# Performance work log

Measured on AMD Instinct MI355X. Metric: run time of the kernel, lower is better.

The kernel has to match this reference:

```python
import jax, jax.numpy as jnp
import numpy as np


def _apply_rope(t, cos, sin):
    # t: [b, s, h, d]; cos/sin: [s, d//2]; interleaved complex rotation
    b, s, h, d = t.shape
    tr = t.reshape(b, s, h, d // 2, 2)
    a, bb = tr[..., 0], tr[..., 1]
    c = cos[None, :, None, :]
    si = sin[None, :, None, :]
    out_r = a * c - bb * si
    out_i = a * si + bb * c
    return jnp.stack([out_r, out_i], axis=-1).reshape(b, s, h, d)


def setup_inputs() -> dict:
    key = jax.random.key(0)
    ks = jax.random.split(key, 10)
    B, S, D = 4, 512, 4096
    H, HKV, HD = 32, 8, 128
    START = 512
    wscale = 0.02  # keep activations in sane range
    x = jax.random.normal(ks[0], (B, S, D), dtype=jnp.float32)
    wq = jax.random.normal(ks[1], (H * HD, D), dtype=jnp.float32) * wscale
    wk = jax.random.normal(ks[2], (HKV * HD, D), dtype=jnp.float32) * wscale
    wv = jax.random.normal(ks[3], (HKV * HD, D), dtype=jnp.float32) * wscale
    wo = jax.random.normal(ks[4], (D, H * HD), dtype=jnp.float32) * wscale
    # RoPE angles for absolute positions [START, START+S)
    theta = 500000.0
    inv_freq = 1.0 / (theta ** (np.arange(0, HD, 2, dtype=np.float32) / HD))
    pos = np.arange(START, START + S, dtype=np.float32)
    ang = pos[:, None] * inv_freq[None, :]  # [S, HD//2]
    freqs_cos = jnp.asarray(np.cos(ang), dtype=jnp.float32)
    freqs_sin = jnp.asarray(np.sin(ang), dtype=jnp.float32)
    cache_k = jax.random.normal(ks[5], (B, START, HKV, HD), dtype=jnp.float32)
    cache_v = jax.random.normal(ks[6], (B, START, HKV, HD), dtype=jnp.float32)
    return {"x": x, "wq": wq, "wk": wk, "wv": wv, "wo": wo,
            "freqs_cos": freqs_cos, "freqs_sin": freqs_sin,
            "cache_k": cache_k, "cache_v": cache_v, "start_pos": START}


def reference(x, wq, wk, wv, wo, freqs_cos, freqs_sin, cache_k, cache_v, start_pos):
    B, S, D = x.shape
    H = wq.shape[0] // 128
    HKV = wk.shape[0] // 128
    HD = 128
    n_rep = H // HKV
    # QKV projections (Linear: y = x @ W^T)
    xq = jnp.einsum('bsd,ed->bse', x, wq).reshape(B, S, H, HD)
    xk = jnp.einsum('bsd,ed->bse', x, wk).reshape(B, S, HKV, HD)
    xv = jnp.einsum('bsd,ed->bse', x, wv).reshape(B, S, HKV, HD)
    # rotary embedding on new q/k
    xq = _apply_rope(xq, freqs_cos, freqs_sin)
    xk = _apply_rope(xk, freqs_cos, freqs_sin)
    # append new k/v to cache -> total kv length T = start_pos + S
    keys = jnp.concatenate([cache_k, xk], axis=1)    # [B, T, HKV, HD]
    values = jnp.concatenate([cache_v, xv], axis=1)  # [B, T, HKV, HD]
    # GQA: repeat kv heads (repeat_interleave along head dim)
    keys = jnp.repeat(keys, n_rep, axis=2)      # [B, T, H, HD]
    values = jnp.repeat(values, n_rep, axis=2)  # [B, T, H, HD]
    scores = jnp.einsum('bqhd,bkhd->bhqk', xq, keys) / jnp.sqrt(jnp.float32(HD))
    # causal mask: query abs pos start_pos+i attends to kv pos <= start_pos+i
    T = start_pos + S
    q_pos = start_pos + jnp.arange(S)
    k_pos = jnp.arange(T)
    mask = k_pos[None, :] <= q_pos[:, None]  # [S, T]
    scores = jnp.where(mask[None, None, :, :], scores, -jnp.inf)
    probs = jax.nn.softmax(scores.astype(jnp.float32), axis=-1).astype(x.dtype)
    out = jnp.einsum('bhqk,bkhd->bqhd', probs, values).reshape(B, S, H * HD)
    return jnp.einsum('bse,de->bsd', out, wo)
```

## Files before the change

### kernel.cpp

```cpp
#include <hip/hip_runtime.h>
#include <hip/hip_bf16.h>


#define B_ 4
#define S_ 512
#define D_ 4096
#define H_ 32
#define HKV_ 8
#define HD_ 128
#define T_ 1024
#define M_ 2048
#define NQKV_ 6144

typedef __attribute__((ext_vector_type(8))) short bf16x8;
typedef __attribute__((ext_vector_type(4))) float f32x4;

#define GLOAD_LDS16(g, l)                                                     \
  __builtin_amdgcn_global_load_lds(                                           \
      (const __attribute__((address_space(1))) void*)(g),                     \
      (__attribute__((address_space(3))) void*)(l), 16, 0, 0)

__global__ void cvt_f32_bf16(const float* __restrict__ in,
                             __hip_bfloat16* __restrict__ out, long n) {
  long i = ((long)blockIdx.x * blockDim.x + threadIdx.x) * 4;
  if (i >= n) return;
  float4 v = *(const float4*)(in + i);
  __hip_bfloat16 t[4] = {__float2bfloat16(v.x), __float2bfloat16(v.y),
                         __float2bfloat16(v.z), __float2bfloat16(v.w)};
  *(uint2*)(out + i) = *(const uint2*)t;
}

__global__ __launch_bounds__(512, 2) void gemm256(
    const __hip_bfloat16* __restrict__ A, const __hip_bfloat16* __restrict__ B,
    float* __restrict__ C, int M, int N, int K, long ldA, long ldB, long ldC) {
  const int nbx = N >> 8;
  const int nwg = nbx * (M >> 8);
  const int lin = blockIdx.x + nbx * blockIdx.y;
  const int cpx = nwg >> 3;
  const int swz = (lin & 7) * cpx + (lin >> 3);
  const int m0 = (swz / nbx) << 8;
  const int n0 = (swz - (swz / nbx) * nbx) << 8;

  const int tid = threadIdx.x;
  const int w = tid >> 6, l = tid & 63;
  const int wm = w >> 2, wn = w & 3;
  const int lr = l & 15, lq = l >> 4;

  __shared__ __align__(16) __hip_bfloat16 smem[8][8192];

  const int rS = w * 16 + (l >> 2);
  const int cS = (l & 3) ^ ((rS >> 1) & 3);
  const __hip_bfloat16* gA = A + (long)(m0 + rS) * ldA + cS * 8;
  const __hip_bfloat16* gB = B + (long)(n0 + rS) * ldB + cS * 8;
  const long stA = 128 * ldA, stB = 128 * ldB;
  const int wofs = w * 512;

  const int cR = (lq ^ ((lr >> 1) & 3)) * 8;
  const int aOff = (wm * 128 + lr) * 32 + cR;
  const int bOff = (wn * 64 + lr) * 32 + cR;

  f32x4 acc[8][4];
#pragma unroll
  for (int i = 0; i < 8; i++)
#pragma unroll
    for (int j = 0; j < 4; j++) acc[i][j] = f32x4{0.f, 0.f, 0.f, 0.f};

  const int nkt = K >> 6;

#define STAGE_A(buf, kh, ko)                                  \
  {                                                           \
    const __hip_bfloat16* g_ = gA + (ko) + (kh) * 32;         \
    __hip_bfloat16* d_ = &smem[(buf) * 4 + (kh)][wofs];       \
    GLOAD_LDS16(g_, d_);                                      \
    GLOAD_LDS16(g_ + stA, d_ + 4096);                         \
  }
#define STAGE_B(buf, kh, ko)                                  \
  {                                                           \
    const __hip_bfloat16* g_ = gB + (ko) + (kh) * 32;         \
    __hip_bfloat16* d_ = &smem[(buf) * 4 + 2 + (kh)][wofs];   \
    GLOAD_LDS16(g_, d_);                                      \
    GLOAD_LDS16(g_ + stB, d_ + 4096);                         \
  }

  STAGE_A(0, 0, 0);
  STAGE_B(0, 0, 0);
  STAGE_A(0, 1, 0);
  STAGE_B(0, 1, 0);
  asm volatile("s_waitcnt vmcnt(4)" ::: "memory");
  __builtin_amdgcn_s_barrier();

  bf16x8 af[4], bfr[4];
  for (int t = 0; t < nkt; ++t) {
    const int b = t & 1;
    int tn = t + 1;
    if (tn == nkt) tn = 0;
    const long ko = (long)tn << 6;
    const __hip_bfloat16* rA0 = &smem[b * 4 + 0][0];
    const __hip_bfloat16* rA1 = &smem[b * 4 + 1][0];
    const __hip_bfloat16* rB0 = &smem[b * 4 + 2][0];
    const __hip_bfloat16* rB1 = &smem[b * 4 + 3][0];

#pragma unroll
    for (int i = 0; i < 4; i++) af[i] = *(const bf16x8*)(rA0 + aOff + i * 512);
#pragma unroll
    for (int j = 0; j < 4; j++) bfr[j] = *(const bf16x8*)(rB0 + bOff + j * 512);
    STAGE_A(b ^ 1, 0, ko);
    __builtin_amdgcn_s_barrier();
    __builtin_amdgcn_s_setprio(1);
#pragma unroll
    for (int i = 0; i < 4; i++)
#pragma unroll
      for (int j = 0; j < 4; j++)
        acc[i][j] = __builtin_amdgcn_mfma_f32_16x16x32_bf16(af[i], bfr[j],
                                                            acc[i][j], 0, 0, 0);
    __builtin_amdgcn_s_setprio(0);
    __builtin_amdgcn_s_barrier();

#pragma unroll
    for (int i = 0; i < 4; i++)
      af[i] = *(const bf16x8*)(rA0 + aOff + (i + 4) * 512);
    STAGE_B(b ^ 1, 0, ko);
    asm volatile("s_waitcnt vmcnt(4)" ::: "memory");
    __builtin_amdgcn_s_barrier();
    __builtin_amdgcn_s_setprio(1);
#pragma unroll
    for (int i = 0; i < 4; i++)
#pragma unroll
      for (int j = 0; j < 4; j++)
        acc[i + 4][j] = __builtin_amdgcn_mfma_f32_16x16x32_bf16(
            af[i], bfr[j], acc[i + 4][j], 0, 0, 0);
    __builtin_amdgcn_s_setprio(0);
    __builtin_amdgcn_s_barrier();

#pragma unroll
    for (int i = 0; i < 4; i++) af[i] = *(const bf16x8*)(rA1 + aOff + i * 512);
#pragma unroll
    for (int j = 0; j < 4; j++) bfr[j] = *(const bf16x8*)(rB1 + bOff + j * 512);
    STAGE_A(b ^ 1, 1, ko);
    __builtin_amdgcn_s_barrier();
    __builtin_amdgcn_s_setprio(1);
#pragma unroll
    for (int i = 0; i < 4; i++)
#pragma unroll
      for (int j = 0; j < 4; j++)
        acc[i][j] = __builtin_amdgcn_mfma_f32_16x16x32_bf16(af[i], bfr[j],
                                                            acc[i][j], 0, 0, 0);
    __builtin_amdgcn_s_setprio(0);
    __builtin_amdgcn_s_barrier();

#pragma unroll
    for (int i = 0; i < 4; i++)
      af[i] = *(const bf16x8*)(rA1 + aOff + (i + 4) * 512);
    STAGE_B(b ^ 1, 1, ko);
    asm volatile("s_waitcnt vmcnt(4)" ::: "memory");
    __builtin_amdgcn_s_barrier();
    __builtin_amdgcn_s_setprio(1);
#pragma unroll
    for (int i = 0; i < 4; i++)
#pragma unroll
      for (int j = 0; j < 4; j++)
        acc[i + 4][j] = __builtin_amdgcn_mfma_f32_16x16x32_bf16(
            af[i], bfr[j], acc[i + 4][j], 0, 0, 0);
    __builtin_amdgcn_s_setprio(0);
    __builtin_amdgcn_s_barrier();
  }
  asm volatile("s_waitcnt vmcnt(0)" ::: "memory");

#undef STAGE_A
#undef STAGE_B

  const int crow = m0 + wm * 128 + lq * 4;
  const int ccol = n0 + wn * 64 + lr;
#pragma unroll
  for (int i = 0; i < 8; i++)
#pragma unroll
    for (int j = 0; j < 4; j++)
#pragma unroll
      for (int r = 0; r < 4; r++)
        C[(long)(crow + i * 16 + r) * ldC + (ccol + j * 16)] = acc[i][j][r];
}

__global__ __launch_bounds__(512, 2) void gemm128(
    const __hip_bfloat16* __restrict__ A, const __hip_bfloat16* __restrict__ B,
    float* __restrict__ C, int M, int N, int K, long ldA, long ldB, long ldC) {
  const int nbx = N >> 8;
  const int nwg = nbx * (M >> 7);
  const int lin = blockIdx.x + nbx * blockIdx.y;
  const int cpx = nwg >> 3;
  const int swz = (lin & 7) * cpx + (lin >> 3);
  const int by = swz / nbx;
  const int m0 = by << 7;
  const int n0 = (swz - by * nbx) << 8;

  const int tid = threadIdx.x;
  const int w = tid >> 6, l = tid & 63;
  const int wm = w >> 2, wn = w & 3;
  const int lr = l & 15, lq = l >> 4;

  __shared__ __align__(16) __hip_bfloat16 smem[2][24576];

  const int rS = w * 16 + (l >> 2);
  const int cS = (l & 3) ^ ((rS >> 1) & 3);
  const __hip_bfloat16* gA = A + (long)(m0 + rS) * ldA + cS * 8;
  const __hip_bfloat16* gB = B + (long)(n0 + rS) * ldB + cS * 8;
  const long stB = 128 * ldB;
  const int wofs = w * 512;

  const int cR = (lq ^ ((lr >> 1) & 3)) * 8;
  const int aOff = (wm * 64 + lr) * 32 + cR;
  const int bOff = (wn * 64 + lr) * 32 + cR;

  f32x4 acc[4][4];
#pragma unroll
  for (int i = 0; i < 4; i++)
#pragma unroll
    for (int j = 0; j < 4; j++) acc[i][j] = f32x4{0.f, 0.f, 0.f, 0.f};

  const int nkt = K >> 6;

#define STAGE128(buf, kh, ko)                                     \
  {                                                               \
    const __hip_bfloat16* ga_ = gA + (ko) + (kh) * 32;            \
    GLOAD_LDS16(ga_, &smem[buf][(kh) * 4096 + wofs]);             \
    const __hip_bfloat16* gb_ = gB + (ko) + (kh) * 32;            \
    __hip_bfloat16* db_ = &smem[buf][8192 + (kh) * 8192 + wofs];  \
    GLOAD_LDS16(gb_, db_);                                        \
    GLOAD_LDS16(gb_ + stB, db_ + 4096);                           \
  }

  STAGE128(0, 0, 0);
  STAGE128(0, 1, 0);
  asm volatile("s_waitcnt vmcnt(3)" ::: "memory");
  __builtin_amdgcn_s_barrier();

  bf16x8 af[4], bfr[4];
  for (int t = 0; t < nkt; ++t) {
    const int b = t & 1;
    int tn = t + 1;
    if (tn == nkt) tn = 0;
    const long ko = (long)tn << 6;
    const __hip_bfloat16* rA = &smem[b][0];
    const __hip_bfloat16* rB = &smem[b][8192];

#pragma unroll
    for (int i = 0; i < 4; i++) af[i] = *(const bf16x8*)(rA + aOff + i * 512);
#pragma unroll
    for (int j = 0; j < 4; j++) bfr[j] = *(const bf16x8*)(rB + bOff + j * 512);
    STAGE128(b ^ 1, 0, ko);
    asm volatile("s_waitcnt vmcnt(3)" ::: "memory");
    __builtin_amdgcn_s_barrier();
    __builtin_amdgcn_s_setprio(1);
#pragma unroll
    for (int i = 0; i < 4; i++)
#pragma unroll
      for (int j = 0; j < 4; j++)
        acc[i][j] = __builtin_amdgcn_mfma_f32_16x16x32_bf16(af[i], bfr[j],
                                                            acc[i][j], 0, 0, 0);
    __builtin_amdgcn_s_setprio(0);
    __builtin_amdgcn_s_barrier();

#pragma unroll
    for (int i = 0; i < 4; i++)
      af[i] = *(const bf16x8*)(rA + 4096 + aOff + i * 512);
#pragma unroll
    for (int j = 0; j < 4; j++)
      bfr[j] = *(const bf16x8*)(rB + 8192 + bOff + j * 512);
    STAGE128(b ^ 1, 1, ko);
    asm volatile("s_waitcnt vmcnt(3)" ::: "memory");
    __builtin_amdgcn_s_barrier();
    __builtin_amdgcn_s_setprio(1);
#pragma unroll
    for (int i = 0; i < 4; i++)
#pragma unroll
      for (int j = 0; j < 4; j++)
        acc[i][j] = __builtin_amdgcn_mfma_f32_16x16x32_bf16(af[i], bfr[j],
                                                            acc[i][j], 0, 0, 0);
    __builtin_amdgcn_s_setprio(0);
    __builtin_amdgcn_s_barrier();
  }
  asm volatile("s_waitcnt vmcnt(0)" ::: "memory");

#undef STAGE128

  const int crow = m0 + wm * 64 + lq * 4;
  const int ccol = n0 + wn * 64 + lr;
#pragma unroll
  for (int i = 0; i < 4; i++)
#pragma unroll
    for (int j = 0; j < 4; j++)
#pragma unroll
      for (int r = 0; r < 4; r++)
        C[(long)(crow + i * 16 + r) * ldC + (ccol + j * 16)] = acc[i][j][r];
}

__global__ __launch_bounds__(256, 2) void flash_attn(
    const __hip_bfloat16* __restrict__ qb,
    const __hip_bfloat16* __restrict__ kb,
    const __hip_bfloat16* __restrict__ vtb,
    __hip_bfloat16* __restrict__ ob) {
  const int qt = 3 - blockIdx.x;
  const int z = blockIdx.y;
  const int b = z >> 5, h = z & 31, kvh = h >> 2;
  const int q0 = qt * 128;
  const int tid = threadIdx.x, wave = tid >> 6, lane = tid & 63;
  const int lr = lane & 15, lq = lane >> 4;
  const int wrow = wave * 32;
  const float scale = 0.08838834764831845f;

  __shared__ __align__(16) __hip_bfloat16 smem[64 * 128 + 128 * 64 + 128 * 72];
  __hip_bfloat16* Ks = smem;
  __hip_bfloat16* Vs = smem + 64 * 128;
  __hip_bfloat16* Ps = smem + 64 * 128 + 128 * 64;
  __hip_bfloat16* Os = smem;

  const __hip_bfloat16* Kz = kb + ((long)(b * 8 + kvh)) * T_ * HD_;
  const __hip_bfloat16* Vz = vtb + ((long)(b * 8 + kvh)) * HD_ * T_;
  const __hip_bfloat16* Qz = qb + ((long)(b * 512 + q0)) * 4096 + h * 128;
  __hip_bfloat16* obz = ob + ((long)(b * 512 + q0)) * 4096 + h * 128;

  bf16x8 qf[2][4];
#pragma unroll
  for (int i = 0; i < 2; i++)
#pragma unroll
    for (int kb4 = 0; kb4 < 4; kb4++)
      qf[i][kb4] = *(const bf16x8*)(Qz + (long)(wrow + i * 16 + lr) * 4096 +
                                    kb4 * 32 + lq * 8);

  int kOff[4], vOff[4];
#pragma unroll
  for (int it = 0; it < 4; it++) {
    int G = it * 256 + tid;
    int t = G >> 4, ck = (G & 15) ^ (t & 7);
    kOff[it] = t * 128 + ck * 8;
    int d = G >> 3, cv = (G & 7) ^ (d & 7);
    vOff[it] = d * 1024 + cv * 8;
  }

  f32x4 O[2][8];
#pragma unroll
  for (int i = 0; i < 2; i++)
#pragma unroll
    for (int j = 0; j < 8; j++) O[i][j] = f32x4{0.f, 0.f, 0.f, 0.f};
  float mst[2][4], lst[2][4];
#pragma unroll
  for (int i = 0; i < 2; i++)
#pragma unroll
    for (int r = 0; r < 4; r++) {
      mst[i][r] = -1e30f;
      lst[i][r] = 0.f;
    }

  const int ntiles = 10 + 2 * qt, fulltiles = 8 + 2 * qt;
  const int hxor = lr & 7;

  for (int kt = 0; kt < ntiles; kt++) {
    const int k0 = kt * 64;
#pragma unroll
    for (int it = 0; it < 4; it++)
      GLOAD_LDS16(Kz + (long)k0 * 128 + kOff[it],
                  Ks + (it * 256 + wave * 64) * 8);
#pragma unroll
    for (int it = 0; it < 4; it++)
      GLOAD_LDS16(Vz + k0 + vOff[it], Vs + (it * 256 + wave * 64) * 8);
    __syncthreads();

    f32x4 s[2][4];
#pragma unroll
    for (int i = 0; i < 2; i++)
#pragma unroll
      for (int j = 0; j < 4; j++) s[i][j] = f32x4{0.f, 0.f, 0.f, 0.f};
#pragma unroll
    for (int kb4 = 0; kb4 < 4; kb4++) {
      bf16x8 kf[4];
#pragma unroll
      for (int j = 0; j < 4; j++)
        kf[j] = *(const bf16x8*)(Ks + (j * 16 + lr) * 128 +
                                 ((kb4 * 4 + lq) ^ hxor) * 8);
#pragma unroll
      for (int i = 0; i < 2; i++)
#pragma unroll
        for (int j = 0; j < 4; j++)
          s[i][j] = __builtin_amdgcn_mfma_f32_16x16x32_bf16(qf[i][kb4], kf[j],
                                                            s[i][j], 0, 0, 0);
    }

    const bool mt = (kt >= fulltiles);
#pragma unroll
    for (int i = 0; i < 2; i++)
#pragma unroll
      for (int j = 0; j < 4; j++)
#pragma unroll
        for (int r = 0; r < 4; r++) {
          float sv = s[i][j][r] * scale;
          if (mt) {
            int key = k0 + j * 16 + lr;
            int qp = 512 + q0 + wrow + i * 16 + lq * 4 + r;
            if (key > qp) sv = -1e30f;
          }
          s[i][j][r] = sv;
        }

    float al[2][4];
#pragma unroll
    for (int i = 0; i < 2; i++)
#pragma unroll
      for (int r = 0; r < 4; r++) {
        float mx = fmaxf(fmaxf(s[i][0][r], s[i][1][r]),
                         fmaxf(s[i][2][r], s[i][3][r]));
        mx = fmaxf(mx, __shfl_xor(mx, 1));
        mx = fmaxf(mx, __shfl_xor(mx, 2));
        mx = fmaxf(mx, __shfl_xor(mx, 4));
        mx = fmaxf(mx, __shfl_xor(mx, 8));
        float mn = fmaxf(mst[i][r], mx);
        al[i][r] = __expf(mst[i][r] - mn);
        mst[i][r] = mn;
      }
#pragma unroll
    for (int i = 0; i < 2; i++)
#pragma unroll
      for (int j = 0; j < 4; j++)
#pragma unroll
        for (int r = 0; r < 4; r++)
          s[i][j][r] = __expf(s[i][j][r] - mst[i][r]);
#pragma unroll
    for (int i = 0; i < 2; i++)
#pragma unroll
      for (int r = 0; r < 4; r++) {
        float sm = s[i][0][r] + s[i][1][r] + s[i][2][r] + s[i][3][r];
        sm += __shfl_xor(sm, 1);
        sm += __shfl_xor(sm, 2);
        sm += __shfl_xor(sm, 4);
        sm += __shfl_xor(sm, 8);
        lst[i][r] = lst[i][r] * al[i][r] + sm;
      }
#pragma unroll
    for (int i = 0; i < 2; i++)
#pragma unroll
      for (int j = 0; j < 8; j++)
#pragma unroll
        for (int r = 0; r < 4; r++) O[i][j][r] *= al[i][r];

#pragma unroll
    for (int i = 0; i < 2; i++)
#pragma unroll
      for (int j = 0; j < 4; j++)
#pragma unroll
        for (int r = 0; r < 4; r++)
          Ps[(wrow + i * 16 + lq * 4 + r) * 72 + j * 16 + lr] =
              __float2bfloat16(s[i][j][r]);

#pragma unroll
    for (int kc = 0; kc < 2; kc++) {
      bf16x8 pa[2];
#pragma unroll
      for (int i = 0; i < 2; i++)
        pa[i] = *(const bf16x8*)(Ps + (wrow + i * 16 + lr) * 72 + kc * 32 +
                                 lq * 8);
      bf16x8 vf[8];
#pragma unroll
      for (int j = 0; j < 8; j++)
        vf[j] = *(const bf16x8*)(Vs + (j * 16 + lr) * 64 +
                                 ((kc * 4 + lq) ^ hxor) * 8);
#pragma unroll
      for (int i = 0; i < 2; i++)
#pragma unroll
        for (int j = 0; j < 8; j++)
          O[i][j] = __builtin_amdgcn_mfma_f32_16x16x32_bf16(pa[i], vf[j],
                                                            O[i][j], 0, 0, 0);
    }
    __syncthreads();
  }

#pragma unroll
  for (int i = 0; i < 2; i++)
#pragma unroll
    for (int r = 0; r < 4; r++) {
      float inv = 1.f / lst[i][r];
#pragma unroll
      for (int j = 0; j < 8; j++)
        Os[(wrow + i * 16 + lq * 4 + r) * 136 + j * 16 + lr] =
            __float2bfloat16(O[i][j][r] * inv);
    }
  __syncthreads();
#pragma unroll
  for (int it = 0; it < 8; it++) {
    int G = it * 256 + tid;
    int m = G >> 4, c = G & 15;
    *(bf16x8*)(obz + (long)m * 4096 + c * 8) =
        *(const bf16x8*)(Os + m * 136 + c * 8);
  }
}

__global__ void rope_kernel(const float* __restrict__ qkv,
                            const float* __restrict__ fcos,
                            const float* __restrict__ fsin,
                            __hip_bfloat16* __restrict__ qb,
                            __hip_bfloat16* __restrict__ kb) {
  int m = blockIdx.y;
  int j = blockIdx.x * blockDim.x + threadIdx.x;
  if (j >= 2560) return;
  int s = m & (S_ - 1);
  long rowbase = (long)m * NQKV_;
  if (j < 2048) {
    int dpair = j & 63;
    float a = qkv[rowbase + 2 * j], bb = qkv[rowbase + 2 * j + 1];
    float c = fcos[s * 64 + dpair], si = fsin[s * 64 + dpair];
    long o = (long)m * 4096 + 2 * j;
    qb[o] = __float2bfloat16(a * c - bb * si);
    qb[o + 1] = __float2bfloat16(a * si + bb * c);
  } else {
    int j2 = j - 2048;
    int kvh = j2 >> 6, dpair = j2 & 63;
    float a = qkv[rowbase + 4096 + 2 * j2], bb = qkv[rowbase + 4096 + 2 * j2 + 1];
    float c = fcos[s * 64 + dpair], si = fsin[s * 64 + dpair];
    int b = m >> 9;
    long o = (((long)(b * HKV_ + kvh)) * T_ + 512 + s) * HD_ + 2 * dpair;
    kb[o] = __float2bfloat16(a * c - bb * si);
    kb[o + 1] = __float2bfloat16(a * si + bb * c);
  }
}

__global__ void kcache_cvt(const float* __restrict__ cache_k,
                           __hip_bfloat16* __restrict__ kb) {
  long i = (long)blockIdx.x * 256 + threadIdx.x;
  if (i >= (long)B_ * HKV_ * 512 * HD_) return;
  int d = i & 127;
  int t = (i >> 7) & 511;
  int kvh = (i >> 16) & 7;
  int b = i >> 19;
  long o = (((long)(b * HKV_ + kvh)) * T_ + t) * HD_ + d;
  kb[o] = __float2bfloat16(
      cache_k[(((long)(b * 512 + t)) * HKV_ + kvh) * HD_ + d]);
}

__global__ void v_transpose(const float* __restrict__ cache_v,
                            const float* __restrict__ qkv,
                            __hip_bfloat16* __restrict__ vtb) {
  __shared__ float tile[32][33];
  int t0 = blockIdx.x * 32, d0 = blockIdx.y * 32;
  int bk = blockIdx.z;
  int b = bk >> 3, kvh = bk & 7;
#pragma unroll
  for (int it = 0; it < 4; it++) {
    int t = t0 + threadIdx.y + it * 8;
    int d = d0 + threadIdx.x;
    float v;
    if (t < 512)
      v = cache_v[(((long)(b * 512 + t)) * HKV_ + kvh) * HD_ + d];
    else
      v = qkv[((long)(b * S_) + (t - 512)) * NQKV_ + 5120 + kvh * HD_ + d];
    tile[threadIdx.y + it * 8][threadIdx.x] = v;
  }
  __syncthreads();
#pragma unroll
  for (int it = 0; it < 4; it++) {
    int d = d0 + threadIdx.y + it * 8;
    int t = t0 + threadIdx.x;
    vtb[((long)bk * HD_ + d) * T_ + t] =
        __float2bfloat16(tile[threadIdx.x][threadIdx.y + it * 8]);
  }
}

extern "C" void kernel_launch(void* const* d_in, const int* in_sizes, int n_in,
                              void* d_out, int out_size, void* d_ws,
                              size_t ws_size, hipStream_t stream) {
  const float* x = (const float*)d_in[0];
  const float* wq = (const float*)d_in[1];
  const float* wk = (const float*)d_in[2];
  const float* wv = (const float*)d_in[3];
  const float* wo = (const float*)d_in[4];
  const float* fcos = (const float*)d_in[5];
  const float* fsin = (const float*)d_in[6];
  const float* cache_k = (const float*)d_in[7];
  const float* cache_v = (const float*)d_in[8];
  float* out = (float*)d_out;

  char* ws = (char*)d_ws;
  const size_t szR0 = (size_t)M_ * 4096 * 2;
  const size_t szR1 = (size_t)NQKV_ * D_ * 2;
  const size_t szR2 = (size_t)M_ * NQKV_ * 4;
  const size_t szKV = (size_t)B_ * HKV_ * T_ * HD_ * 2;

  size_t R0 = 0;
  size_t R1 = R0 + szR0;
  size_t R2 = R1 + szR1;
  size_t R3 = R2 + szR2;
  size_t R4 = R3 + szKV;

  __hip_bfloat16* xb = (__hip_bfloat16*)(ws + R0);
  __hip_bfloat16* wqkvb = (__hip_bfloat16*)(ws + R1);
  float* qkvf = (float*)(ws + R2);
  __hip_bfloat16* kb = (__hip_bfloat16*)(ws + R3);
  __hip_bfloat16* vtb = (__hip_bfloat16*)(ws + R4);

  dim3 blk(256);

  cvt_f32_bf16<<<(M_ * (long)D_ / 4 + 255) / 256, blk, 0, stream>>>(
      x, xb, (long)M_ * D_);
  cvt_f32_bf16<<<((long)D_ * D_ / 4 + 255) / 256, blk, 0, stream>>>(
      wq, wqkvb, (long)D_ * D_);
  cvt_f32_bf16<<<((long)1024 * D_ / 4 + 255) / 256, blk, 0, stream>>>(
      wk, wqkvb + (long)4096 * D_, (long)1024 * D_);
  cvt_f32_bf16<<<((long)1024 * D_ / 4 + 255) / 256, blk, 0, stream>>>(
      wv, wqkvb + (long)5120 * D_, (long)1024 * D_);

  gemm256<<<dim3(NQKV_ / 256, M_ / 256), dim3(512), 0, stream>>>(
      xb, wqkvb, qkvf, M_, NQKV_, D_, D_, D_, NQKV_);

  __hip_bfloat16* qb = xb;
  rope_kernel<<<dim3(10, M_), blk, 0, stream>>>(qkvf, fcos, fsin, qb, kb);

  kcache_cvt<<<((long)B_ * HKV_ * 512 * HD_ + 255) / 256, blk, 0, stream>>>(
      cache_k, kb);
  v_transpose<<<dim3(T_ / 32, HD_ / 32, B_ * HKV_), dim3(32, 8), 0, stream>>>(
      cache_v, qkvf, vtb);

  __hip_bfloat16* wob = wqkvb;
  cvt_f32_bf16<<<((long)D_ * D_ / 4 + 255) / 256, blk, 0, stream>>>(
      wo, wob, (long)D_ * D_);

  __hip_bfloat16* ob = xb;
  flash_attn<<<dim3(4, B_ * H_), blk, 0, stream>>>(qb, kb, vtb, ob);

  gemm128<<<dim3(D_ / 256, M_ / 128), dim3(512), 0, stream>>>(
      ob, wob, out, M_, D_, D_, D_, D_, D_);
}
```

Before: 508.7 us.

## Triple-buffer GEMM shared memory with prefetch distance two and one barrier per tile

```diff
diff --git a/kernel.cpp b/kernel.cpp
--- a/kernel.cpp
+++ b/kernel.cpp
@@ -197,7 +197,7 @@
   const int wm = w >> 2, wn = w & 3;
   const int lr = l & 15, lq = l >> 4;
 
-  __shared__ __align__(16) __hip_bfloat16 smem[2][24576];
+  __shared__ __align__(16) __hip_bfloat16 smem[3][24576];
 
   const int rS = w * 16 + (l >> 2);
   const int cS = (l & 3) ^ ((rS >> 1) & 3);
@@ -218,37 +218,38 @@
 
   const int nkt = K >> 6;
 
-#define STAGE128(buf, kh, ko)                                     \
-  {                                                               \
-    const __hip_bfloat16* ga_ = gA + (ko) + (kh) * 32;            \
-    GLOAD_LDS16(ga_, &smem[buf][(kh) * 4096 + wofs]);             \
-    const __hip_bfloat16* gb_ = gB + (ko) + (kh) * 32;            \
-    __hip_bfloat16* db_ = &smem[buf][8192 + (kh) * 8192 + wofs];  \
-    GLOAD_LDS16(gb_, db_);                                        \
-    GLOAD_LDS16(gb_ + stB, db_ + 4096);                           \
-  }
-
-  STAGE128(0, 0, 0);
-  STAGE128(0, 1, 0);
-  asm volatile("s_waitcnt vmcnt(3)" ::: "memory");
+#define STAGEF(buf, ko)                                            \
+  {                                                                \
+    const __hip_bfloat16* ga_ = gA + (ko);                         \
+    GLOAD_LDS16(ga_, &smem[buf][wofs]);                            \
+    GLOAD_LDS16(ga_ + 32, &smem[buf][4096 + wofs]);                \
+    const __hip_bfloat16* gb_ = gB + (ko);                         \
+    GLOAD_LDS16(gb_, &smem[buf][8192 + wofs]);                     \
+    GLOAD_LDS16(gb_ + stB, &smem[buf][12288 + wofs]);              \
+    GLOAD_LDS16(gb_ + 32, &smem[buf][16384 + wofs]);               \
+    GLOAD_LDS16(gb_ + stB + 32, &smem[buf][20480 + wofs]);         \
+  }
+
+  STAGEF(0, 0);
+  STAGEF(1, 64);
+  asm volatile("s_waitcnt vmcnt(6)" ::: "memory");
   __builtin_amdgcn_s_barrier();
 
+  int bc = 0, b1 = 1, b2 = 2;
   bf16x8 af[4], bfr[4];
   for (int t = 0; t < nkt; ++t) {
-    const int b = t & 1;
-    int tn = t + 1;
-    if (tn == nkt) tn = 0;
-    const long ko = (long)tn << 6;
-    const __hip_bfloat16* rA = &smem[b][0];
-    const __hip_bfloat16* rB = &smem[b][8192];
+    int t2 = t + 2;
+    if (t2 >= nkt) t2 -= nkt;
+    const long ko2 = (long)t2 << 6;
+    STAGEF(b2, ko2);
+
+    const __hip_bfloat16* rA = &smem[bc][0];
+    const __hip_bfloat16* rB = &smem[bc][8192];
 
 #pragma unroll
     for (int i = 0; i < 4; i++) af[i] = *(const bf16x8*)(rA + aOff + i * 512);
 #pragma unroll
     for (int j = 0; j < 4; j++) bfr[j] = *(const bf16x8*)(rB + bOff + j * 512);
-    STAGE128(b ^ 1, 0, ko);
-    asm volatile("s_waitcnt vmcnt(3)" ::: "memory");
-    __builtin_amdgcn_s_barrier();
     __builtin_amdgcn_s_setprio(1);
 #pragma unroll
     for (int i = 0; i < 4; i++)
@@ -257,7 +258,6 @@
         acc[i][j] = __builtin_amdgcn_mfma_f32_16x16x32_bf16(af[i], bfr[j],
                                                             acc[i][j], 0, 0, 0);
     __builtin_amdgcn_s_setprio(0);
-    __builtin_amdgcn_s_barrier();
 
 #pragma unroll
     for (int i = 0; i < 4; i++)
@@ -265,9 +265,6 @@
 #pragma unroll
     for (int j = 0; j < 4; j++)
       bfr[j] = *(const bf16x8*)(rB + 8192 + bOff + j * 512);
-    STAGE128(b ^ 1, 1, ko);
-    asm volatile("s_waitcnt vmcnt(3)" ::: "memory");
-    __builtin_amdgcn_s_barrier();
     __builtin_amdgcn_s_setprio(1);
 #pragma unroll
     for (int i = 0; i < 4; i++)
@@ -276,11 +273,17 @@
         acc[i][j] = __builtin_amdgcn_mfma_f32_16x16x32_bf16(af[i], bfr[j],
                                                             acc[i][j], 0, 0, 0);
     __builtin_amdgcn_s_setprio(0);
-    __builtin_amdgcn_s_barrier();
+
+    asm volatile("s_waitcnt lgkmcnt(0)" ::: "memory");
+    __builtin_amdgcn_sched_barrier(0);
+    asm volatile("s_waitcnt vmcnt(6)" ::: "memory");
+    __builtin_amdgcn_s_barrier();
+
+    int tmp = bc; bc = b1; b1 = b2; b2 = tmp;
   }
   asm volatile("s_waitcnt vmcnt(0)" ::: "memory");
 
-#undef STAGE128
+#undef STAGEF
 
   const int crow = m0 + wm * 64 + lq * 4;
   const int ccol = n0 + wn * 64 + lr;
```

After: 496.0 us. -2.5%, faster.
